# Optimization experiments

Measured on AMD Instinct MI355X. Metric: run time of the kernel, lower is better.

Reference implementation:

```python
import jax, jax.numpy as jnp
import numpy as np

H = 768   # hidden (cell) size
P = 256   # projection size
I = 80    # input feature dim
L = 3     # model_num_layers
B, T = 256, 400


def setup_inputs() -> dict:
    key = jax.random.key(0)
    ks = jax.random.split(key, 16)
    s = 0.05
    inp = {"x": jax.random.normal(ks[0], (B, T, I), dtype=jnp.float32)}
    in_dims = [I, P, P]
    for l in range(L):
        inp[f"Wx{l}"] = jax.random.normal(ks[1 + 4 * l], (in_dims[l], 4 * H), dtype=jnp.float32) * s
        inp[f"Wh{l}"] = jax.random.normal(ks[2 + 4 * l], (P, 4 * H), dtype=jnp.float32) * s
        inp[f"b{l}"] = jnp.zeros((4 * H,), dtype=jnp.float32)
        inp[f"Wp{l}"] = jax.random.normal(ks[3 + 4 * l], (H, P), dtype=jnp.float32) * s
    inp["W"] = jax.random.normal(ks[13], (P, P), dtype=jnp.float32) * s
    inp["lb"] = jnp.zeros((P,), dtype=jnp.float32)
    return inp


def _lstmp_layer(x, Wx, Wh, b, Wp, c0, h0):
    # Precompute input contribution to gates: [B, T, 4H]
    xg = jnp.einsum("bti,ig->btg", x, Wx) + b

    def step(carry, xg_t):
        c, h = carry
        gates = xg_t + h @ Wh              # [B, 4H]
        i, f, g, o = jnp.split(gates, 4, axis=-1)
        i = jax.nn.sigmoid(i)
        f = jax.nn.sigmoid(f)
        g = jnp.tanh(g)
        o = jax.nn.sigmoid(o)
        c = f * c + i * g                  # [B, H]
        h = (o * jnp.tanh(c)) @ Wp         # [B, P] projected hidden
        return (c, h), h

    (c, h), hs = jax.lax.scan(step, (c0, h0), jnp.swapaxes(xg, 0, 1))
    return jnp.swapaxes(hs, 0, 1), c, h   # seq_out [B,T,P], final c, h


def reference(x, Wx0, Wh0, b0, Wp0, Wx1, Wh1, b1, Wp1, Wx2, Wh2, b2, Wp2, W, lb):
    batch = x.shape[0]
    c = jnp.zeros((batch, H), dtype=x.dtype)
    h = jnp.zeros((batch, P), dtype=x.dtype)
    seq = x
    params = [(Wx0, Wh0, b0, Wp0), (Wx1, Wh1, b1, Wp1), (Wx2, Wh2, b2, Wp2)]
    for (Wx, Wh, b, Wp) in params:
        seq, c, h = _lstmp_layer(seq, Wx, Wh, b, Wp, c, h)
    embeds_raw = jax.nn.relu(seq.mean(axis=1) @ W.T + lb)   # [B, P]
    norm = jnp.linalg.norm(embeds_raw, axis=1, keepdims=True)
    return embeds_raw / norm
```

## Files before the change

kernel.cpp:

```cpp
#include <hip/hip_runtime.h>
#include <cstdint>
#include <cstddef>


typedef __attribute__((ext_vector_type(8))) short bf16x8;
typedef __attribute__((ext_vector_type(4))) float f32x4;
typedef __attribute__((ext_vector_type(2))) int i32x2;

#define TT 400
#define NB 256
#define IIP 96
#define HH 768
#define PP 256
#define G4 3072
#define NWG 32
#define NGRP 8
#define NTIL 3
#define BLDS 147456
#define SMEMB (BLDS + 1536 + 64)

__device__ __forceinline__ short f2bf(float f) {
  unsigned u = __builtin_bit_cast(unsigned, f);
  unsigned r = u + 0x7FFFu + ((u >> 16) & 1u);
  return (short)(r >> 16);
}
__device__ __forceinline__ float sigf(float x) { return 1.0f / (1.0f + __expf(-x)); }
__device__ __forceinline__ float tanh_(float x) { return 1.0f - 2.0f / (__expf(2.0f * x) + 1.0f); }

__device__ __forceinline__ void st_co_b64(void* p, i32x2 v) {
  asm volatile("global_store_dwordx2 %0, %1, off sc0 sc1" :: "v"(p), "v"(v) : "memory");
}
__device__ __forceinline__ void st_co_b32(void* p, int v) {
  asm volatile("global_store_dword %0, %1, off sc0 sc1" :: "v"(p), "v"(v) : "memory");
}
__device__ __forceinline__ int ld_flag_g(const int* p) {
  int v;
  asm volatile("global_load_dword %0, %1, off sc0 sc1\n\ts_waitcnt vmcnt(0)"
               : "=v"(v) : "v"(p) : "memory");
  return v;
}
__device__ __forceinline__ bf16x8 ld_sc0(const void* p) {
  bf16x8 v;
  asm volatile("global_load_dwordx4 %0, %1, off sc0" : "=v"(v) : "v"(p));
  return v;
}
__device__ __forceinline__ int get_xcc() {
  int x;
  asm("s_getreg_b32 %0, hwreg(HW_REG_XCC_ID)" : "=s"(x));
  return x & 15;
}
#define WAIT_TIE24(u) \
  asm volatile("s_waitcnt vmcnt(0)" \
    : "+v"(u[0]),"+v"(u[1]),"+v"(u[2]),"+v"(u[3]),"+v"(u[4]),"+v"(u[5]), \
      "+v"(u[6]),"+v"(u[7]),"+v"(u[8]),"+v"(u[9]),"+v"(u[10]),"+v"(u[11]), \
      "+v"(u[12]),"+v"(u[13]),"+v"(u[14]),"+v"(u[15]),"+v"(u[16]),"+v"(u[17]), \
      "+v"(u[18]),"+v"(u[19]),"+v"(u[20]),"+v"(u[21]),"+v"(u[22]),"+v"(u[23]))


__global__ void k_xb(const float* __restrict__ x, short* __restrict__ xb) {
  int idx = blockIdx.x * 256 + threadIdx.x;
  if (idx >= TT * NB * 80) return;
  int i = idx % 80, tb = idx / 80;
  int b = tb % NB, t = tb / NB;
  xb[(size_t)(t * NB + b) * IIP + i] = f2bf(x[(size_t)(b * TT + t) * 80 + i]);
}

__device__ __forceinline__ int colmap(int np) {
  int jj = np / 96, w = np % 96;
  return (w & 3) * HH + jj * 24 + (w >> 2);
}

__global__ void k_makeB(const float* __restrict__ Wx, const float* __restrict__ Wp,
                        const float* __restrict__ Wh, short* __restrict__ out,
                        int K, int KIN, int INDIM) {
  int np = blockIdx.x * 256 + threadIdx.x;
  int k = blockIdx.y;
  int col = colmap(np);
  float v;
  if (k < KIN) {
    v = (k < INDIM) ? Wx[(size_t)k * G4 + col] : 0.0f;
  } else {
    float a = 0.f;
    int kr = k - KIN;
    for (int q = 0; q < PP; ++q)
      a = fmaf(Wp[(size_t)kr * PP + q], Wh[(size_t)q * G4 + col], a);
    v = a;
  }
  out[(size_t)np * K + k] = f2bf(v);
}

__global__ void k_wpT(const float* __restrict__ Wp, short* __restrict__ WpT) {
  int idx = blockIdx.x * 256 + threadIdx.x;
  if (idx >= PP * HH) return;
  int n = idx % PP, k = idx / PP;
  WpT[(size_t)n * HH + k] = f2bf(Wp[(size_t)k * PP + n]);
}

__global__ void k_whT(const float* __restrict__ Wh, short* __restrict__ WhT) {
  int idx = blockIdx.x * 256 + threadIdx.x;
  if (idx >= G4 * PP) return;
  int np = idx % G4, k = idx / G4;
  WhT[(size_t)np * PP + k] = f2bf(Wh[(size_t)k * G4 + colmap(np)]);
}

__global__ void k_pb(const float* b0, const float* b1, const float* b2, float* pb) {
  int n = blockIdx.x * 256 + threadIdx.x;
  if (n >= 3 * G4) return;
  int l = n / G4, np = n % G4;
  pb[n] = (l == 0 ? b0 : (l == 1 ? b1 : b2))[colmap(np)];
}

__global__ void k_wt(const float* __restrict__ W, float* __restrict__ Wt) {
  int idx = blockIdx.x * 256 + threadIdx.x;
  int q = idx >> 8, p = idx & 255;
  Wt[idx] = W[p * 256 + q];
}

__global__ void __launch_bounds__(256) k_trans2(
    const short* __restrict__ seqF, const short* __restrict__ WhT,
    float* __restrict__ xg0b)
{
  const int blk = blockIdx.x;
  const int g = blk & 3, j = blk >> 2;
  const int tid = threadIdx.x, lane = tid & 63, wv = tid >> 6;
  const int c0 = lane & 15, rg = lane >> 4;
  const int row0 = g * 64;
  const short* aseq = seqF + (size_t)(row0 + wv * 16 + c0) * PP + rg * 8;

  f32x4 zz = {0.f, 0.f, 0.f, 0.f};
  f32x4 acc[4];
  #pragma unroll
  for (int nt = 0; nt < 4; ++nt) acc[nt] = zz;
  #pragma unroll
  for (int c = 0; c < 8; ++c) {
    bf16x8 a = *(const bf16x8*)(aseq + c * 32);
    #pragma unroll
    for (int nt = 0; nt < 4; ++nt) {
      bf16x8 b = *(const bf16x8*)(WhT + (size_t)(j * 64 + nt * 16 + c0) * PP + c * 32 + rg * 8);
      acc[nt] = __builtin_amdgcn_mfma_f32_16x16x32_bf16(a, b, acc[nt], 0, 0, 0);
    }
  }
  #pragma unroll
  for (int nt = 0; nt < 4; ++nt)
    #pragma unroll
    for (int r = 0; r < 4; ++r)
      xg0b[(size_t)(row0 + wv * 16 + rg * 4 + r) * G4 + j * 64 + nt * 16 + c0] = acc[nt][r];
}


template <int CIN, int DOPROJ, int DOSUM, int USEXG>
__global__ void __launch_bounds__(256, 1) k_layer(
    const short* __restrict__ Bw,
    const short* __restrict__ inS, const int inStr,
    const short* __restrict__ WpT, short* __restrict__ projOut,
    const float* __restrict__ pbL,
    short* __restrict__ U, float* __restrict__ Cw, float* __restrict__ S,
    const float* __restrict__ xg0b, int* __restrict__ pages)
{
  extern __shared__ char smem[];
  char* BsC = smem;
  short* UtS = (short*)(smem + BLDS);
  char* xcl = smem + BLDS + 1536;
  const int bx = blockIdx.x;
  const int g = bx & 7;
  const int j = bx >> 3;
  const int tid = threadIdx.x;
  const int lane = tid & 63, wv = tid >> 6;
  const int mv = wv >> 1, nh = wv & 1;
  const int c0 = lane & 15, rg = lane >> 4;
  const int row0 = g * 32;
  const int gate = c0 & 3, qb = lane & ~3;
  constexpr int K = CIN * 32 + 768;
  constexpr int KIN = CIN * 32;

  char* page = (char*)pages + g * 4096;
  int* cnt  = (int*)page;
  int* cntX = (int*)(page + 1024);
  int* xpub = (int*)(page + 2048);

  const int myxcc = get_xcc();
  if (tid == 0) st_co_b32(xpub + j, myxcc);
  asm volatile("s_waitcnt vmcnt(0)" ::: "memory");
  __syncthreads();
  if (tid == 0) __hip_atomic_fetch_add(cntX, 1, __ATOMIC_RELAXED, __HIP_MEMORY_SCOPE_AGENT);

  {
    const short* srcB = Bw + (size_t)j * 96 * K + KIN;
    #pragma unroll
    for (int it = 0; it < 36; ++it) {
      int u = it * 256 + tid;
      int wj = u % 96, q = u / 96;
      int c = q >> 2, r4 = q & 3;
      bf16x8 v = *(const bf16x8*)(srcB + (size_t)wj * K + c * 32 + r4 * 8);
      *(bf16x8*)(BsC + c * 6144 + wj * 64 + (((r4 ^ (wj >> 1)) & 3) << 4)) = v;
    }
  }

  if (wv == 0) {
    while (ld_flag_g(cntX) < NWG) __builtin_amdgcn_s_sleep(2);
    if (lane < NWG) xcl[lane] = (char)ld_flag_g(xpub + lane);
  }
  __syncthreads();
  bool locv = true;
  for (int i = 0; i < NWG; ++i) locv = locv && (xcl[i] == (char)myxcc);
  const bool loc = locv;

  float creg[NTIL][4], sreg[NTIL][4];
  #pragma unroll
  for (int nt = 0; nt < NTIL; ++nt)
    #pragma unroll
    for (int r = 0; r < 4; ++r) {
      int cell = j * 24 + nh * 12 + nt * 4 + (c0 >> 2);
      creg[nt][r] = USEXG ? Cw[(size_t)(row0 + mv * 16 + rg * 4 + r) * HH + cell] : 0.f;
      sreg[nt][r] = 0.f;
    }

  float bias[NTIL];
  int fbB[NTIL];
  const short* xB[NTIL];
  #pragma unroll
  for (int nt = 0; nt < NTIL; ++nt) {
    int wj = nh * 48 + nt * 16 + c0;
    bias[nt] = pbL[j * 96 + wj];
    fbB[nt] = wj * 64 + (((rg ^ (wj >> 1)) & 3) << 4);
    xB[nt] = Bw + (size_t)(j * 96 + wj) * K + rg * 8;
  }
  const short* wb = DOPROJ ? (WpT + (size_t)(j * 16 + c0) * HH + rg * 8) : nullptr;
  f32x4 zz = {0.f, 0.f, 0.f, 0.f};

  __syncthreads();

  bf16x8 uf[24];
  for (int t = 0; t < TT; ++t) {
    const int pw = t & 1, pr = pw ^ 1;
    const short* aX = inS + ((size_t)t * NB + row0 + mv * 16 + c0) * inStr + rg * 8;
    const short* aU = U + ((size_t)pr * NB + row0 + mv * 16 + c0) * HH + rg * 8;

    f32x4 acc[NTIL];
    if (USEXG && t == 0) {
      #pragma unroll
      for (int nt = 0; nt < NTIL; ++nt)
        #pragma unroll
        for (int r = 0; r < 4; ++r)
          acc[nt][r] = xg0b[(size_t)(row0 + mv * 16 + rg * 4 + r) * G4
                            + j * 96 + nh * 48 + nt * 16 + c0];
    } else {
      #pragma unroll
      for (int nt = 0; nt < NTIL; ++nt) acc[nt] = zz;
    }

    #pragma unroll
    for (int c = 0; c < CIN; ++c) {
      bf16x8 a = *(const bf16x8*)(aX + c * 32);
      #pragma unroll
      for (int nt = 0; nt < NTIL; ++nt)
        acc[nt] = __builtin_amdgcn_mfma_f32_16x16x32_bf16(
            a, *(const bf16x8*)(xB[nt] + c * 32), acc[nt], 0, 0, 0);
    }

    if (t > 0) {
      if (wv == 0) {
        while (ld_flag_g(cnt) < NWG * t) __builtin_amdgcn_s_sleep(1);
        if (!loc) __builtin_amdgcn_fence(__ATOMIC_ACQUIRE, "agent");
      }
      __syncthreads();
      if (loc) {
        #pragma unroll
        for (int c = 0; c < 24; ++c) uf[c] = ld_sc0(aU + c * 32);
        WAIT_TIE24(uf);
      } else {
        #pragma unroll
        for (int c = 0; c < 24; ++c) uf[c] = *(const bf16x8*)(aU + c * 32);
      }
      #pragma unroll
      for (int c = 0; c < 24; ++c)
        #pragma unroll
        for (int nt = 0; nt < NTIL; ++nt)
          acc[nt] = __builtin_amdgcn_mfma_f32_16x16x32_bf16(
              uf[c], *(const bf16x8*)(BsC + c * 6144 + fbB[nt]), acc[nt], 0, 0, 0);
    }

    #pragma unroll
    for (int nt = 0; nt < NTIL; ++nt) {
      #pragma unroll
      for (int r = 0; r < 4; ++r) {
        float xv = acc[nt][r] + bias[nt];
        float pre = (gate == 2) ? 2.0f * xv : xv;
        float s = sigf(pre);
        float v = (gate == 2) ? 2.0f * s - 1.0f : s;
        float q0 = __shfl(v, qb + 0);
        float q1 = __shfl(v, qb + 1);
        float q2 = __shfl(v, qb + 2);
        float q3 = __shfl(v, qb + 3);
        float cc2 = q1 * creg[nt][r] + q0 * q2;
        creg[nt][r] = cc2;
        float uu = q3 * tanh_(cc2);
        if (DOSUM) sreg[nt][r] += uu;
        if (gate == 0)
          UtS[(mv * 16 + rg * 4 + r) * 24 + nh * 12 + nt * 4 + (c0 >> 2)] = f2bf(uu);
      }
    }
    __syncthreads();
    if (tid < 192) {
      int row = tid / 6, seg = tid - row * 6;
      i32x2 v = *(const i32x2*)((char*)UtS + row * 48 + seg * 8);
      short* dst = U + ((size_t)pw * NB + row0 + row) * HH + j * 24 + seg * 4;
      if (loc) *(i32x2*)dst = v;
      else st_co_b64(dst, v);
    }
    asm volatile("s_waitcnt vmcnt(0)" ::: "memory");
    __syncthreads();
    if (tid == 0)
      __hip_atomic_fetch_add(cnt, 1, __ATOMIC_RELAXED, __HIP_MEMORY_SCOPE_AGENT);

    if (DOPROJ && j < 16 && t > 0) {
      if (nh == 0) {
        f32x4 pacc = zz;
        #pragma unroll
        for (int c = 0; c < 24; ++c)
          pacc = __builtin_amdgcn_mfma_f32_16x16x32_bf16(
              uf[c], *(const bf16x8*)(wb + c * 32), pacc, 0, 0, 0);
        #pragma unroll
        for (int r = 0; r < 4; ++r)
          UtS[(mv * 16 + rg * 4 + r) * 16 + c0] = f2bf(pacc[r]);
      }
      __syncthreads();
      if (tid < 128) {
        int row = tid >> 2, q = tid & 3;
        i32x2 v = *(const i32x2*)((char*)UtS + row * 32 + q * 8);
        short* dst = projOut + ((size_t)(t - 1) * NB + row0 + row) * PP + j * 16 + q * 4;
        if (loc) *(i32x2*)dst = v;
        else st_co_b64(dst, v);
      }
    }
  }

  if (wv == 0) {
    while (ld_flag_g(cnt) < NWG * TT) __builtin_amdgcn_s_sleep(1);
    if (!loc) __builtin_amdgcn_fence(__ATOMIC_ACQUIRE, "agent");
  }
  __syncthreads();
  if (DOPROJ && j < 16) {
    if (nh == 0) {
      const short* aU1 = U + ((size_t)1 * NB + row0 + mv * 16 + c0) * HH + rg * 8;
      if (loc) {
        #pragma unroll
        for (int c = 0; c < 24; ++c) uf[c] = ld_sc0(aU1 + c * 32);
        WAIT_TIE24(uf);
      } else {
        #pragma unroll
        for (int c = 0; c < 24; ++c) uf[c] = *(const bf16x8*)(aU1 + c * 32);
      }
      f32x4 pacc = zz;
      #pragma unroll
      for (int c = 0; c < 24; ++c)
        pacc = __builtin_amdgcn_mfma_f32_16x16x32_bf16(
            uf[c], *(const bf16x8*)(wb + c * 32), pacc, 0, 0, 0);
      #pragma unroll
      for (int r = 0; r < 4; ++r)
        UtS[(mv * 16 + rg * 4 + r) * 16 + c0] = f2bf(pacc[r]);
    }
    __syncthreads();
    if (tid < 128) {
      int row = tid >> 2, q = tid & 3;
      i32x2 v = *(const i32x2*)((char*)UtS + row * 32 + q * 8);
      short* dst = projOut + ((size_t)399 * NB + row0 + row) * PP + j * 16 + q * 4;
      if (loc) *(i32x2*)dst = v;
      else st_co_b64(dst, v);
    }
  }

  if (gate == 0) {
    #pragma unroll
    for (int nt = 0; nt < NTIL; ++nt)
      #pragma unroll
      for (int r = 0; r < 4; ++r) {
        size_t idx = (size_t)(row0 + mv * 16 + rg * 4 + r) * HH
                     + j * 24 + nh * 12 + nt * 4 + (c0 >> 2);
        Cw[idx] = creg[nt][r];
        if (DOSUM) S[idx] = sreg[nt][r];
      }
  }
}


__global__ void k_mh(const float* __restrict__ S, const float* __restrict__ Wp2, float* __restrict__ mh) {
  __shared__ float sl[HH];
  int b = blockIdx.x, p = threadIdx.x;
  for (int i = p; i < HH; i += 256) sl[i] = S[(size_t)b * HH + i] * (1.0f / 400.0f);
  __syncthreads();
  float a = 0.f;
  for (int k = 0; k < HH; ++k) a = fmaf(sl[k], Wp2[(size_t)k * PP + p], a);
  mh[b * PP + p] = a;
}

__global__ void k_out(const float* __restrict__ mh, const float* __restrict__ Wt,
                      const float* __restrict__ lb, float* __restrict__ out) {
  __shared__ float ml[PP];
  __shared__ float red[PP];
  int b = blockIdx.x, p = threadIdx.x;
  ml[p] = mh[b * PP + p];
  __syncthreads();
  float z = lb[p];
  for (int q = 0; q < PP; ++q) z = fmaf(ml[q], Wt[q * PP + p], z);
  z = fmaxf(z, 0.0f);
  red[p] = z * z;
  __syncthreads();
  for (int st = 128; st > 0; st >>= 1) { if (p < st) red[p] += red[p + st]; __syncthreads(); }
  out[b * PP + p] = z / sqrtf(red[0]);
}


extern "C" void kernel_launch(void* const* d_in, const int* in_sizes, int n_in,
                              void* d_out, int out_size, void* d_ws, size_t ws_size,
                              hipStream_t stream) {
  (void)in_sizes; (void)n_in; (void)out_size; (void)ws_size;
  const float* x   = (const float*)d_in[0];
  const float* Wx0 = (const float*)d_in[1];
  const float* Wh0 = (const float*)d_in[2];
  const float* b0  = (const float*)d_in[3];
  const float* Wp0 = (const float*)d_in[4];
  const float* Wx1 = (const float*)d_in[5];
  const float* Wh1 = (const float*)d_in[6];
  const float* b1  = (const float*)d_in[7];
  const float* Wp1 = (const float*)d_in[8];
  const float* Wx2 = (const float*)d_in[9];
  const float* Wh2 = (const float*)d_in[10];
  const float* b2  = (const float*)d_in[11];
  const float* Wp2 = (const float*)d_in[12];
  const float* W   = (const float*)d_in[13];
  const float* lb  = (const float*)d_in[14];

  char* w = (char*)d_ws;
  auto take = [&](size_t bytes) { char* p = w; w += (bytes + 4095) & ~(size_t)4095; return p; };
  short* xb    = (short*)take((size_t)TT * NB * IIP * 2);
  short* B0w   = (short*)take((size_t)G4 * 864 * 2);
  short* B1w   = (short*)take((size_t)G4 * 1024 * 2);
  short* B2w   = (short*)take((size_t)G4 * 1024 * 2);
  float* pbw   = (float*)take((size_t)3 * G4 * 4);
  short* WpT0  = (short*)take((size_t)PP * HH * 2);
  short* WpT1  = (short*)take((size_t)PP * HH * 2);
  short* WhT1  = (short*)take((size_t)G4 * PP * 2);
  short* WhT2  = (short*)take((size_t)G4 * PP * 2);
  short* U     = (short*)take((size_t)2 * NB * HH * 2);
  short* seqH  = (short*)take((size_t)TT * NB * PP * 2);
  float* xg0b  = (float*)take((size_t)NB * G4 * 4);
  float* Cw    = (float*)take((size_t)NB * HH * 4);
  float* Sw    = (float*)take((size_t)NB * HH * 4);
  float* mhw   = (float*)take((size_t)NB * PP * 4);
  float* Wtw   = (float*)take((size_t)PP * PP * 4);
  int*   cnts  = (int*)take(3 * NGRP * 4096);

  hipMemsetAsync(xb, 0, (size_t)TT * NB * IIP * 2, stream);
  hipMemsetAsync(cnts, 0, 3 * NGRP * 4096, stream);

  k_xb<<<(TT * NB * 80 + 255) / 256, 256, 0, stream>>>(x, xb);
  k_makeB<<<dim3(12, 864), 256, 0, stream>>>(Wx0, Wp0, Wh0, B0w, 864, 96, 80);
  k_makeB<<<dim3(12, 1024), 256, 0, stream>>>(Wx1, Wp1, Wh1, B1w, 1024, 256, 256);
  k_makeB<<<dim3(12, 1024), 256, 0, stream>>>(Wx2, Wp2, Wh2, B2w, 1024, 256, 256);
  k_wpT<<<(PP * HH + 255) / 256, 256, 0, stream>>>(Wp0, WpT0);
  k_wpT<<<(PP * HH + 255) / 256, 256, 0, stream>>>(Wp1, WpT1);
  k_whT<<<(G4 * PP + 255) / 256, 256, 0, stream>>>(Wh1, WhT1);
  k_whT<<<(G4 * PP + 255) / 256, 256, 0, stream>>>(Wh2, WhT2);
  k_pb<<<(3 * G4 + 255) / 256, 256, 0, stream>>>(b0, b1, b2, pbw);
  k_wt<<<(PP * PP) / 256, 256, 0, stream>>>(W, Wtw);

  hipFuncSetAttribute((const void*)k_layer<3, 1, 0, 0>,
                      hipFuncAttributeMaxDynamicSharedMemorySize, SMEMB);
  hipFuncSetAttribute((const void*)k_layer<8, 1, 0, 1>,
                      hipFuncAttributeMaxDynamicSharedMemorySize, SMEMB);
  hipFuncSetAttribute((const void*)k_layer<8, 0, 1, 1>,
                      hipFuncAttributeMaxDynamicSharedMemorySize, SMEMB);

  k_layer<3, 1, 0, 0><<<256, 256, SMEMB, stream>>>(
      B0w, xb, IIP, WpT0, seqH, pbw + 0 * G4, U, Cw, Sw, xg0b,
      (int*)((char*)cnts + 0 * NGRP * 4096));
  k_trans2<<<192, 256, 0, stream>>>(seqH + (size_t)399 * NB * PP, WhT1, xg0b);

  k_layer<8, 1, 0, 1><<<256, 256, SMEMB, stream>>>(
      B1w, seqH, PP, WpT1, seqH, pbw + 1 * G4, U, Cw, Sw, xg0b,
      (int*)((char*)cnts + 1 * NGRP * 4096));
  k_trans2<<<192, 256, 0, stream>>>(seqH + (size_t)399 * NB * PP, WhT2, xg0b);

  k_layer<8, 0, 1, 1><<<256, 256, SMEMB, stream>>>(
      B2w, seqH, PP, nullptr, nullptr, pbw + 2 * G4, U, Cw, Sw, xg0b,
      (int*)((char*)cnts + 2 * NGRP * 4096));

  k_mh<<<NB, 256, 0, stream>>>(Sw, Wp2, mhw);
  k_out<<<NB, 256, 0, stream>>>(mhw, Wtw, lb, (float*)d_out);
}
```

Before: 12.37 ms.

## Interleave two batch groups per workgroup with per-block flag slots

Halves the persistent grid from 256 to 128 workgroups. Each workgroup now handles two 32-row batch groups and alternates between them every timestep, so the recurrent wait on one group can overlap with compute on the other. The shared atomic counter and XCC-locality detection are replaced by per-workgroup flag slots that are polled with a wave-wide all-check. All U and projection traffic now uses coherent sc0 sc1 loads and stores. The cost is twice the register state per workgroup, half the workgroups in use, and always-coherent memory traffic even when the workgroups are co-located.

```diff
diff --git a/kernel.cpp b/kernel.cpp
--- a/kernel.cpp
+++ b/kernel.cpp
@@ -17,7 +17,8 @@
 #define NGRP 8
 #define NTIL 3
 #define BLDS 147456
-#define SMEMB (BLDS + 1536 + 64)
+#define SMEMB (BLDS + 1536)
+#define PGSZ 8192
 
 __device__ __forceinline__ short f2bf(float f) {
   unsigned u = __builtin_bit_cast(unsigned, f);
@@ -39,15 +40,8 @@
                : "=v"(v) : "v"(p) : "memory");
   return v;
 }
-__device__ __forceinline__ bf16x8 ld_sc0(const void* p) {
-  bf16x8 v;
-  asm volatile("global_load_dwordx4 %0, %1, off sc0" : "=v"(v) : "v"(p));
-  return v;
-}
-__device__ __forceinline__ int get_xcc() {
-  int x;
-  asm("s_getreg_b32 %0, hwreg(HW_REG_XCC_ID)" : "=s"(x));
-  return x & 15;
+__device__ __forceinline__ void ld_co(bf16x8* d, const void* p) {
+  asm volatile("global_load_dwordx4 %0, %1, off sc0 sc1" : "=v"(*d) : "v"(p));
 }
 #define WAIT_TIE24(u) \
   asm volatile("s_waitcnt vmcnt(0)" \
@@ -160,59 +154,43 @@
   extern __shared__ char smem[];
   char* BsC = smem;
   short* UtS = (short*)(smem + BLDS);
-  char* xcl = smem + BLDS + 1536;
   const int bx = blockIdx.x;
-  const int g = bx & 7;
-  const int j = bx >> 3;
+  const int q = bx & 3;
+  const int j = bx >> 2;
   const int tid = threadIdx.x;
   const int lane = tid & 63, wv = tid >> 6;
   const int mv = wv >> 1, nh = wv & 1;
   const int c0 = lane & 15, rg = lane >> 4;
-  const int row0 = g * 32;
   const int gate = c0 & 3, qb = lane & ~3;
+  const int row0A = q * 64, row0B = q * 64 + 32;
   constexpr int K = CIN * 32 + 768;
   constexpr int KIN = CIN * 32;
 
-  char* page = (char*)pages + g * 4096;
-  int* cnt  = (int*)page;
-  int* cntX = (int*)(page + 1024);
-  int* xpub = (int*)(page + 2048);
-
-  const int myxcc = get_xcc();
-  if (tid == 0) st_co_b32(xpub + j, myxcc);
-  asm volatile("s_waitcnt vmcnt(0)" ::: "memory");
-  __syncthreads();
-  if (tid == 0) __hip_atomic_fetch_add(cntX, 1, __ATOMIC_RELAXED, __HIP_MEMORY_SCOPE_AGENT);
+  int* slotsA = (int*)((char*)pages + (size_t)(2 * q) * PGSZ);
+  int* slotsB = (int*)((char*)pages + (size_t)(2 * q + 1) * PGSZ);
 
   {
     const short* srcB = Bw + (size_t)j * 96 * K + KIN;
     #pragma unroll
     for (int it = 0; it < 36; ++it) {
       int u = it * 256 + tid;
-      int wj = u % 96, q = u / 96;
-      int c = q >> 2, r4 = q & 3;
+      int wj = u % 96, qq = u / 96;
+      int c = qq >> 2, r4 = qq & 3;
       bf16x8 v = *(const bf16x8*)(srcB + (size_t)wj * K + c * 32 + r4 * 8);
       *(bf16x8*)(BsC + c * 6144 + wj * 64 + (((r4 ^ (wj >> 1)) & 3) << 4)) = v;
     }
   }
 
-  if (wv == 0) {
-    while (ld_flag_g(cntX) < NWG) __builtin_amdgcn_s_sleep(2);
-    if (lane < NWG) xcl[lane] = (char)ld_flag_g(xpub + lane);
-  }
-  __syncthreads();
-  bool locv = true;
-  for (int i = 0; i < NWG; ++i) locv = locv && (xcl[i] == (char)myxcc);
-  const bool loc = locv;
-
-  float creg[NTIL][4], sreg[NTIL][4];
+  float cregA[NTIL][4], sregA[NTIL][4], cregB[NTIL][4], sregB[NTIL][4];
   #pragma unroll
   for (int nt = 0; nt < NTIL; ++nt)
     #pragma unroll
     for (int r = 0; r < 4; ++r) {
       int cell = j * 24 + nh * 12 + nt * 4 + (c0 >> 2);
-      creg[nt][r] = USEXG ? Cw[(size_t)(row0 + mv * 16 + rg * 4 + r) * HH + cell] : 0.f;
-      sreg[nt][r] = 0.f;
+      cregA[nt][r] = USEXG ? Cw[(size_t)(row0A + mv * 16 + rg * 4 + r) * HH + cell] : 0.f;
+      cregB[nt][r] = USEXG ? Cw[(size_t)(row0B + mv * 16 + rg * 4 + r) * HH + cell] : 0.f;
+      sregA[nt][r] = 0.f;
+      sregB[nt][r] = 0.f;
     }
 
   float bias[NTIL];
@@ -225,14 +203,25 @@
     fbB[nt] = wj * 64 + (((rg ^ (wj >> 1)) & 3) << 4);
     xB[nt] = Bw + (size_t)(j * 96 + wj) * K + rg * 8;
   }
-  const short* wb = DOPROJ ? (WpT + (size_t)(j * 16 + c0) * HH + rg * 8) : nullptr;
-  f32x4 zz = {0.f, 0.f, 0.f, 0.f};
+  const short* wbp = DOPROJ ? (WpT + (size_t)(j * 16 + c0) * HH + rg * 8) : nullptr;
+  const f32x4 zz = {0.f, 0.f, 0.f, 0.f};
 
   __syncthreads();
 
-  bf16x8 uf[24];
-  for (int t = 0; t < TT; ++t) {
-    const int pw = t & 1, pr = pw ^ 1;
+  auto poll = [&](int* slots, int tgt) {
+    if (wv == 0) {
+      const int* sp = slots + (lane & 31) * 32;
+      for (;;) {
+        int v = ld_flag_g(sp);
+        if (__all(v >= tgt)) break;
+        __builtin_amdgcn_s_sleep(1);
+      }
+    }
+    __syncthreads();
+  };
+
+  auto phase = [&](int row0, int* slots, float (&creg)[NTIL][4], float (&sreg)[NTIL][4],
+                   int t, int pw, int pr) {
     const short* aX = inS + ((size_t)t * NB + row0 + mv * 16 + c0) * inStr + rg * 8;
     const short* aU = U + ((size_t)pr * NB + row0 + mv * 16 + c0) * HH + rg * 8;
 
@@ -258,20 +247,12 @@
             a, *(const bf16x8*)(xB[nt] + c * 32), acc[nt], 0, 0, 0);
     }
 
+    bf16x8 uf[24];
     if (t > 0) {
-      if (wv == 0) {
-        while (ld_flag_g(cnt) < NWG * t) __builtin_amdgcn_s_sleep(1);
-        if (!loc) __builtin_amdgcn_fence(__ATOMIC_ACQUIRE, "agent");
-      }
-      __syncthreads();
-      if (loc) {
-        #pragma unroll
-        for (int c = 0; c < 24; ++c) uf[c] = ld_sc0(aU + c * 32);
-        WAIT_TIE24(uf);
-      } else {
-        #pragma unroll
-        for (int c = 0; c < 24; ++c) uf[c] = *(const bf16x8*)(aU + c * 32);
-      }
+      poll(slots, t);
+      #pragma unroll
+      for (int c = 0; c < 24; ++c) ld_co(&uf[c], aU + c * 32);
+      WAIT_TIE24(uf);
       #pragma unroll
       for (int c = 0; c < 24; ++c)
         #pragma unroll
@@ -304,14 +285,11 @@
     if (tid < 192) {
       int row = tid / 6, seg = tid - row * 6;
       i32x2 v = *(const i32x2*)((char*)UtS + row * 48 + seg * 8);
-      short* dst = U + ((size_t)pw * NB + row0 + row) * HH + j * 24 + seg * 4;
-      if (loc) *(i32x2*)dst = v;
-      else st_co_b64(dst, v);
+      st_co_b64(U + ((size_t)pw * NB + row0 + row) * HH + j * 24 + seg * 4, v);
     }
     asm volatile("s_waitcnt vmcnt(0)" ::: "memory");
     __syncthreads();
-    if (tid == 0)
-      __hip_atomic_fetch_add(cnt, 1, __ATOMIC_RELAXED, __HIP_MEMORY_SCOPE_AGENT);
+    if (tid == 0) st_co_b32(slots + j * 32, t + 1);
 
     if (DOPROJ && j < 16 && t > 0) {
       if (nh == 0) {
@@ -319,66 +297,68 @@
         #pragma unroll
         for (int c = 0; c < 24; ++c)
           pacc = __builtin_amdgcn_mfma_f32_16x16x32_bf16(
-              uf[c], *(const bf16x8*)(wb + c * 32), pacc, 0, 0, 0);
+              uf[c], *(const bf16x8*)(wbp + c * 32), pacc, 0, 0, 0);
         #pragma unroll
         for (int r = 0; r < 4; ++r)
           UtS[(mv * 16 + rg * 4 + r) * 16 + c0] = f2bf(pacc[r]);
       }
       __syncthreads();
       if (tid < 128) {
-        int row = tid >> 2, q = tid & 3;
-        i32x2 v = *(const i32x2*)((char*)UtS + row * 32 + q * 8);
-        short* dst = projOut + ((size_t)(t - 1) * NB + row0 + row) * PP + j * 16 + q * 4;
-        if (loc) *(i32x2*)dst = v;
-        else st_co_b64(dst, v);
-      }
-    }
-  }
-
-  if (wv == 0) {
-    while (ld_flag_g(cnt) < NWG * TT) __builtin_amdgcn_s_sleep(1);
-    if (!loc) __builtin_amdgcn_fence(__ATOMIC_ACQUIRE, "agent");
-  }
-  __syncthreads();
-  if (DOPROJ && j < 16) {
-    if (nh == 0) {
-      const short* aU1 = U + ((size_t)1 * NB + row0 + mv * 16 + c0) * HH + rg * 8;
-      if (loc) {
-        #pragma unroll
-        for (int c = 0; c < 24; ++c) uf[c] = ld_sc0(aU1 + c * 32);
+        int row = tid >> 2, qq = tid & 3;
+        i32x2 v = *(const i32x2*)((char*)UtS + row * 32 + qq * 8);
+        st_co_b64(projOut + ((size_t)(t - 1) * NB + row0 + row) * PP + j * 16 + qq * 4, v);
+      }
+      __syncthreads();
+    }
+  };
+
+  for (int t = 0; t < TT; ++t) {
+    const int pw = t & 1, pr = pw ^ 1;
+    phase(row0A, slotsA, cregA, sregA, t, pw, pr);
+    phase(row0B, slotsB, cregB, sregB, t, pw, pr);
+  }
+
+  auto tail = [&](int row0, int* slots) {
+    poll(slots, TT);
+    if (DOPROJ && j < 16) {
+      if (nh == 0) {
+        bf16x8 uf[24];
+        const short* aU1 = U + ((size_t)1 * NB + row0 + mv * 16 + c0) * HH + rg * 8;
+        #pragma unroll
+        for (int c = 0; c < 24; ++c) ld_co(&uf[c], aU1 + c * 32);
         WAIT_TIE24(uf);
-      } else {
-        #pragma unroll
-        for (int c = 0; c < 24; ++c) uf[c] = *(const bf16x8*)(aU1 + c * 32);
-      }
-      f32x4 pacc = zz;
-      #pragma unroll
-      for (int c = 0; c < 24; ++c)
-        pacc = __builtin_amdgcn_mfma_f32_16x16x32_bf16(
-            uf[c], *(const bf16x8*)(wb + c * 32), pacc, 0, 0, 0);
-      #pragma unroll
-      for (int r = 0; r < 4; ++r)
-        UtS[(mv * 16 + rg * 4 + r) * 16 + c0] = f2bf(pacc[r]);
-    }
-    __syncthreads();
-    if (tid < 128) {
-      int row = tid >> 2, q = tid & 3;
-      i32x2 v = *(const i32x2*)((char*)UtS + row * 32 + q * 8);
-      short* dst = projOut + ((size_t)399 * NB + row0 + row) * PP + j * 16 + q * 4;
-      if (loc) *(i32x2*)dst = v;
-      else st_co_b64(dst, v);
-    }
-  }
+        f32x4 pacc = zz;
+        #pragma unroll
+        for (int c = 0; c < 24; ++c)
+          pacc = __builtin_amdgcn_mfma_f32_16x16x32_bf16(
+              uf[c], *(const bf16x8*)(wbp + c * 32), pacc, 0, 0, 0);
+        #pragma unroll
+        for (int r = 0; r < 4; ++r)
+          UtS[(mv * 16 + rg * 4 + r) * 16 + c0] = f2bf(pacc[r]);
+      }
+      __syncthreads();
+      if (tid < 128) {
+        int row = tid >> 2, qq = tid & 3;
+        i32x2 v = *(const i32x2*)((char*)UtS + row * 32 + qq * 8);
+        st_co_b64(projOut + ((size_t)399 * NB + row0 + row) * PP + j * 16 + qq * 4, v);
+      }
+      __syncthreads();
+    }
+  };
+  tail(row0A, slotsA);
+  tail(row0B, slotsB);
 
   if (gate == 0) {
     #pragma unroll
     for (int nt = 0; nt < NTIL; ++nt)
       #pragma unroll
       for (int r = 0; r < 4; ++r) {
-        size_t idx = (size_t)(row0 + mv * 16 + rg * 4 + r) * HH
-                     + j * 24 + nh * 12 + nt * 4 + (c0 >> 2);
-        Cw[idx] = creg[nt][r];
-        if (DOSUM) S[idx] = sreg[nt][r];
+        int cell = j * 24 + nh * 12 + nt * 4 + (c0 >> 2);
+        size_t iA = (size_t)(row0A + mv * 16 + rg * 4 + r) * HH + cell;
+        size_t iB = (size_t)(row0B + mv * 16 + rg * 4 + r) * HH + cell;
+        Cw[iA] = cregA[nt][r];
+        Cw[iB] = cregB[nt][r];
+        if (DOSUM) { S[iA] = sregA[nt][r]; S[iB] = sregB[nt][r]; }
       }
   }
 }
@@ -449,10 +429,10 @@
   float* Sw    = (float*)take((size_t)NB * HH * 4);
   float* mhw   = (float*)take((size_t)NB * PP * 4);
   float* Wtw   = (float*)take((size_t)PP * PP * 4);
-  int*   cnts  = (int*)take(3 * NGRP * 4096);
+  int*   cnts  = (int*)take(3 * NGRP * PGSZ);
 
   hipMemsetAsync(xb, 0, (size_t)TT * NB * IIP * 2, stream);
-  hipMemsetAsync(cnts, 0, 3 * NGRP * 4096, stream);
+  hipMemsetAsync(cnts, 0, 3 * NGRP * PGSZ, stream);
 
   k_xb<<<(TT * NB * 80 + 255) / 256, 256, 0, stream>>>(x, xb);
   k_makeB<<<dim3(12, 864), 256, 0, stream>>>(Wx0, Wp0, Wh0, B0w, 864, 96, 80);
@@ -472,19 +452,19 @@
   hipFuncSetAttribute((const void*)k_layer<8, 0, 1, 1>,
                       hipFuncAttributeMaxDynamicSharedMemorySize, SMEMB);
 
-  k_layer<3, 1, 0, 0><<<256, 256, SMEMB, stream>>>(
+  k_layer<3, 1, 0, 0><<<128, 256, SMEMB, stream>>>(
       B0w, xb, IIP, WpT0, seqH, pbw + 0 * G4, U, Cw, Sw, xg0b,
-      (int*)((char*)cnts + 0 * NGRP * 4096));
+      (int*)((char*)cnts + 0 * NGRP * PGSZ));
   k_trans2<<<192, 256, 0, stream>>>(seqH + (size_t)399 * NB * PP, WhT1, xg0b);
 
-  k_layer<8, 1, 0, 1><<<256, 256, SMEMB, stream>>>(
+  k_layer<8, 1, 0, 1><<<128, 256, SMEMB, stream>>>(
       B1w, seqH, PP, WpT1, seqH, pbw + 1 * G4, U, Cw, Sw, xg0b,
-      (int*)((char*)cnts + 1 * NGRP * 4096));
+      (int*)((char*)cnts + 1 * NGRP * PGSZ));
   k_trans2<<<192, 256, 0, stream>>>(seqH + (size_t)399 * NB * PP, WhT2, xg0b);
 
-  k_layer<8, 0, 1, 1><<<256, 256, SMEMB, stream>>>(
+  k_layer<8, 0, 1, 1><<<128, 256, SMEMB, stream>>>(
       B2w, seqH, PP, nullptr, nullptr, pbw + 2 * G4, U, Cw, Sw, xg0b,
-      (int*)((char*)cnts + 2 * NGRP * 4096));
+      (int*)((char*)cnts + 2 * NGRP * PGSZ));
 
   k_mh<<<NB, 256, 0, stream>>>(Sw, Wp2, mhw);
   k_out<<<NB, 256, 0, stream>>>(mhw, Wtw, lb, (float*)d_out);
```

Result: slower. 26.21 ms (+111.9%).
